# Kernel tuning notes

Measured on AMD Instinct MI355X. Metric: run time of the kernel, lower is better.

Reference implementation:

```python
import jax, jax.numpy as jnp
import numpy as np

MAX_ABS = 1.0          # assumed get_max_abs('T')
DT = 0.01              # forward default dt
TWO_PI = 2.0 * np.pi
B, D, N = 4096, 2048, 4096


def setup_inputs() -> dict:
    key = jax.random.key(0)
    k0, k1 = jax.random.split(key, 2)
    x = jax.random.normal(k0, (B, D), dtype=jnp.float32)
    # nn.Linear params
    W = jax.random.normal(k1, (N, D), dtype=jnp.float32) * (1.0 / np.sqrt(D))
    b = jnp.zeros((N,), dtype=jnp.float32)
    # oscillator params (as initialized in __init__)
    amplitude = jnp.ones((N,), dtype=jnp.float32)
    frequency = jnp.ones((N,), dtype=jnp.float32)
    phase_offset = jnp.zeros((N,), dtype=jnp.float32)
    damping = jnp.full((N,), 0.01, dtype=jnp.float32)
    return {"x": x, "W": W, "b": b, "amplitude": amplitude,
            "frequency": frequency, "phase_offset": phase_offset,
            "damping": damping}


def reference(x, W, b, amplitude, frequency, phase_offset, damping):
    # driving force: [B, N]
    force = x @ W.T + b
    omega_sq = (TWO_PI * frequency) ** 2  # [N]
    # t starts at 0 and is incremented ONCE per forward call
    t = DT

    def step(carry, f):
        state, vel = carry
        accel = -omega_sq * state - damping * vel + f
        vel = vel + accel * DT
        state = state + vel * DT
        return (state, vel), state

    init = (jnp.zeros((N,), x.dtype), jnp.zeros((N,), x.dtype))
    (_, _), states = jax.lax.scan(step, init, force)  # states: [B, N]

    # sinusoid term is identical for every batch step (t fixed within forward)
    osc = amplitude * jnp.sin(TWO_PI * frequency * t + phase_offset)  # [N]
    out = jnp.clip(states + osc, -MAX_ABS, MAX_ABS)
    return out
```

## Files before the change

### kernel.cpp

```cpp
#include <hip/hip_runtime.h>
#include <hip/hip_bf16.h>
#include <math.h>

#define MDIM 4096
#define KDIM 2048
#define NDIM 4096
#define DT   0.01f
#define TWO_PI_F 6.283185307179586f
#define CH 64
#define CL 64

typedef __attribute__((ext_vector_type(8))) short bf16x8;
typedef __attribute__((ext_vector_type(4))) float f32x4;

__device__ __forceinline__ unsigned short f2bf(float f) {
  unsigned int u = __float_as_uint(f);
  u += 0x7FFFu + ((u >> 16) & 1u);
  return (unsigned short)(u >> 16);
}
__device__ __forceinline__ float bf2f(unsigned short u) {
  return __uint_as_float(((unsigned int)u) << 16);
}

__global__ void cast2_bf16_kernel(const float* __restrict__ s0,
                                  unsigned short* __restrict__ d0,
                                  const float* __restrict__ s1,
                                  unsigned short* __restrict__ d1,
                                  int n4each) {
  int i = blockIdx.x * blockDim.x + threadIdx.x;
  const float4* sp;
  ushort4* dp;
  int j;
  if (i < n4each) { sp = (const float4*)s0; dp = (ushort4*)d0; j = i; }
  else            { sp = (const float4*)s1; dp = (ushort4*)d1; j = i - n4each; }
  float4 v = sp[j];
  ushort4 o;
  o.x = f2bf(v.x); o.y = f2bf(v.y); o.z = f2bf(v.z); o.w = f2bf(v.w);
  dp[j] = o;
}

__global__ __launch_bounds__(256, 2) void gemm_bt_kernel(
    const unsigned short* __restrict__ A,
    const unsigned short* __restrict__ Bm,
    const float* __restrict__ bias,
    unsigned short* __restrict__ C) {
  __shared__ __align__(16) unsigned short sA[128 * 32];
  __shared__ __align__(16) unsigned short sB[128 * 32];

  const int tid  = threadIdx.x;
  const int lane = tid & 63;
  const int wave = tid >> 6;
  const int wr = wave >> 1;
  const int wc = wave & 1;
  const int q  = lane >> 4;
  const int lm = lane & 15;

  const int bM = blockIdx.x * 128;
  const int bN = blockIdx.y * 128;

  f32x4 acc[4][4];
#pragma unroll
  for (int i = 0; i < 4; i++)
#pragma unroll
    for (int j = 0; j < 4; j++) acc[i][j] = (f32x4){0.f, 0.f, 0.f, 0.f};

  const int idx0 = tid;
  const int idx1 = tid + 256;
  const int r0 = idx0 >> 2, g0 = idx0 & 3;
  const int r1 = idx1 >> 2, g1 = idx1 & 3;
  const int dst0 = r0 * 32 + ((g0 ^ ((r0 >> 1) & 3)) * 8);
  const int dst1 = r1 * 32 + ((g1 ^ ((r1 >> 1) & 3)) * 8);
  const unsigned short* gA0 = A  + (size_t)(bM + r0) * KDIM + g0 * 8;
  const unsigned short* gA1 = A  + (size_t)(bM + r1) * KDIM + g1 * 8;
  const unsigned short* gB0 = Bm + (size_t)(bN + r0) * KDIM + g0 * 8;
  const unsigned short* gB1 = Bm + (size_t)(bN + r1) * KDIM + g1 * 8;

  const int rq = (q ^ ((lm >> 1) & 3)) * 8;

  for (int k0 = 0; k0 < KDIM; k0 += 32) {
    uint4 av0 = *(const uint4*)(gA0 + k0);
    uint4 av1 = *(const uint4*)(gA1 + k0);
    uint4 bv0 = *(const uint4*)(gB0 + k0);
    uint4 bv1 = *(const uint4*)(gB1 + k0);
    __syncthreads();
    *(uint4*)&sA[dst0] = av0;
    *(uint4*)&sA[dst1] = av1;
    *(uint4*)&sB[dst0] = bv0;
    *(uint4*)&sB[dst1] = bv1;
    __syncthreads();

    bf16x8 af[4], bfr[4];
#pragma unroll
    for (int mt = 0; mt < 4; mt++)
      af[mt]  = *(const bf16x8*)&sA[(wr * 64 + mt * 16 + lm) * 32 + rq];
#pragma unroll
    for (int nt = 0; nt < 4; nt++)
      bfr[nt] = *(const bf16x8*)&sB[(wc * 64 + nt * 16 + lm) * 32 + rq];

#pragma unroll
    for (int mt = 0; mt < 4; mt++)
#pragma unroll
      for (int nt = 0; nt < 4; nt++)
        acc[mt][nt] = __builtin_amdgcn_mfma_f32_16x16x32_bf16(
            af[mt], bfr[nt], acc[mt][nt], 0, 0, 0);
  }

#pragma unroll
  for (int nt = 0; nt < 4; nt++) {
    const int col = bN + wc * 64 + nt * 16 + lm;
    const float bz = bias[col];
#pragma unroll
    for (int mt = 0; mt < 4; mt++) {
      const int row0 = bM + wr * 64 + mt * 16 + q * 4;
#pragma unroll
      for (int r = 0; r < 4; r++)
        C[(size_t)(row0 + r) * NDIM + col] = f2bf(acc[mt][nt][r] + bz);
    }
  }
}

__global__ void scan_pass1(const unsigned short* __restrict__ force,
                           const float* __restrict__ freq,
                           const float* __restrict__ damp,
                           float* __restrict__ chunkS,
                           float* __restrict__ chunkV) {
  int gid = blockIdx.x * blockDim.x + threadIdx.x;
  int n4 = gid & (NDIM / 4 - 1);
  int c  = gid >> 10;
  int n  = n4 * 4;
  float4 fr = *(const float4*)&freq[n];
  float4 dv = *(const float4*)&damp[n];
  float osq[4] = {TWO_PI_F * fr.x, TWO_PI_F * fr.y, TWO_PI_F * fr.z, TWO_PI_F * fr.w};
  float dp[4]  = {dv.x, dv.y, dv.z, dv.w};
  float s[4] = {0.f, 0.f, 0.f, 0.f}, v[4] = {0.f, 0.f, 0.f, 0.f};
#pragma unroll
  for (int j = 0; j < 4; j++) osq[j] *= osq[j];
  const unsigned short* fp = force + (size_t)c * CL * NDIM + n;
#pragma unroll 4
  for (int i = 0; i < CL; i++) {
    ushort4 fv = *(const ushort4*)&fp[(size_t)i * NDIM];
    float f[4] = {bf2f(fv.x), bf2f(fv.y), bf2f(fv.z), bf2f(fv.w)};
#pragma unroll
    for (int j = 0; j < 4; j++) {
      float a = -osq[j] * s[j] - dp[j] * v[j] + f[j];
      v[j] += a * DT;
      s[j] += v[j] * DT;
    }
  }
  *(float4*)&chunkS[c * NDIM + n] = (float4){s[0], s[1], s[2], s[3]};
  *(float4*)&chunkV[c * NDIM + n] = (float4){v[0], v[1], v[2], v[3]};
}

__global__ void scan_pass2(const float* __restrict__ chunkS,
                           const float* __restrict__ chunkV,
                           const float* __restrict__ freq,
                           const float* __restrict__ damp,
                           float* __restrict__ carryS,
                           float* __restrict__ carryV) {
  int n = blockIdx.x * blockDim.x + threadIdx.x;
  float om = TWO_PI_F * freq[n];
  float osq = om * om;
  float dp = damp[n];
  float a00 = 1.f - osq * DT * DT, a01 = DT * (1.f - dp * DT);
  float a10 = -osq * DT,           a11 = 1.f - dp * DT;
#pragma unroll
  for (int i = 0; i < 6; i++) {
    float b00 = a00 * a00 + a01 * a10;
    float b01 = a00 * a01 + a01 * a11;
    float b10 = a10 * a00 + a11 * a10;
    float b11 = a10 * a01 + a11 * a11;
    a00 = b00; a01 = b01; a10 = b10; a11 = b11;
  }
  float cs = 0.f, cv = 0.f;
#pragma unroll 8
  for (int c = 0; c < CH; c++) {
    carryS[c * NDIM + n] = cs;
    carryV[c * NDIM + n] = cv;
    float ls = chunkS[c * NDIM + n];
    float lv = chunkV[c * NDIM + n];
    float ns = a00 * cs + a01 * cv + ls;
    float nv = a10 * cs + a11 * cv + lv;
    cs = ns; cv = nv;
  }
}

__global__ void scan_pass3(const unsigned short* __restrict__ force,
                           const float* __restrict__ amp,
                           const float* __restrict__ freq,
                           const float* __restrict__ phase,
                           const float* __restrict__ damp,
                           const float* __restrict__ carryS,
                           const float* __restrict__ carryV,
                           float* __restrict__ out) {
  int gid = blockIdx.x * blockDim.x + threadIdx.x;
  int n4 = gid & (NDIM / 4 - 1);
  int c  = gid >> 10;
  int n  = n4 * 4;
  float4 fr = *(const float4*)&freq[n];
  float4 dv = *(const float4*)&damp[n];
  float4 am = *(const float4*)&amp[n];
  float4 ph = *(const float4*)&phase[n];
  float om[4] = {TWO_PI_F * fr.x, TWO_PI_F * fr.y, TWO_PI_F * fr.z, TWO_PI_F * fr.w};
  float dp[4] = {dv.x, dv.y, dv.z, dv.w};
  float osq[4], osc[4], s[4], v[4];
  float amv[4] = {am.x, am.y, am.z, am.w};
  float phv[4] = {ph.x, ph.y, ph.z, ph.w};
#pragma unroll
  for (int j = 0; j < 4; j++) {
    osq[j] = om[j] * om[j];
    osc[j] = amv[j] * sinf(om[j] * DT + phv[j]);
  }
  float4 csv = *(const float4*)&carryS[c * NDIM + n];
  float4 cvv = *(const float4*)&carryV[c * NDIM + n];
  s[0] = csv.x; s[1] = csv.y; s[2] = csv.z; s[3] = csv.w;
  v[0] = cvv.x; v[1] = cvv.y; v[2] = cvv.z; v[3] = cvv.w;
  const unsigned short* fp = force + (size_t)c * CL * NDIM + n;
  float* op = out + (size_t)c * CL * NDIM + n;
#pragma unroll 4
  for (int i = 0; i < CL; i++) {
    ushort4 fv = *(const ushort4*)&fp[(size_t)i * NDIM];
    float f[4] = {bf2f(fv.x), bf2f(fv.y), bf2f(fv.z), bf2f(fv.w)};
    float o[4];
#pragma unroll
    for (int j = 0; j < 4; j++) {
      float a = -osq[j] * s[j] - dp[j] * v[j] + f[j];
      v[j] += a * DT;
      s[j] += v[j] * DT;
      o[j] = fminf(1.f, fmaxf(-1.f, s[j] + osc[j]));
    }
    *(float4*)&op[(size_t)i * NDIM] = (float4){o[0], o[1], o[2], o[3]};
  }
}

extern "C" void kernel_launch(void* const* d_in, const int* in_sizes, int n_in,
                              void* d_out, int out_size, void* d_ws, size_t ws_size,
                              hipStream_t stream) {
  const float* x     = (const float*)d_in[0];
  const float* W     = (const float*)d_in[1];
  const float* bias  = (const float*)d_in[2];
  const float* amp   = (const float*)d_in[3];
  const float* freq  = (const float*)d_in[4];
  const float* phase = (const float*)d_in[5];
  const float* damp  = (const float*)d_in[6];

  unsigned short* xbf   = (unsigned short*)d_ws;
  unsigned short* wbf   = xbf + (size_t)MDIM * KDIM;
  unsigned short* force = wbf + (size_t)NDIM * KDIM;
  float* chunkS = (float*)d_ws;
  float* chunkV = chunkS + CH * NDIM;
  float* carryS = chunkV + CH * NDIM;
  float* carryV = carryS + CH * NDIM;

  const int n4each = MDIM * KDIM / 4;
  cast2_bf16_kernel<<<(2 * n4each + 255) / 256, 256, 0, stream>>>(
      x, xbf, W, wbf, n4each);

  dim3 gg(MDIM / 128, NDIM / 128);
  gemm_bt_kernel<<<gg, 256, 0, stream>>>(xbf, wbf, bias, force);

  scan_pass1<<<CH * NDIM / 4 / 256, 256, 0, stream>>>(force, freq, damp,
                                                      chunkS, chunkV);
  scan_pass2<<<NDIM / 256, 256, 0, stream>>>(chunkS, chunkV, freq, damp,
                                             carryS, carryV);
  scan_pass3<<<CH * NDIM / 4 / 256, 256, 0, stream>>>(
      force, amp, freq, phase, damp, carryS, carryV, (float*)d_out);
}
```

Before: 229.1 us.

## Fuse per-chunk oscillator scan into GEMM epilogue and merge carry pass

The GEMM epilogue now stages each wave's 64x64 tile in shared memory, runs the zero-initial-state oscillator recurrence down each column, and writes the partial states plus chunk-final state and velocity. A single follow-up kernel composes the chunk carries using the 64-step transition matrix, which is built by squaring the one-step matrix six times. It then adds the propagated homogeneous response to the partial states, applies the sinusoid and clips. This drops the separate force pass and the carry kernel, cutting a full read of the force matrix and two launches. The trade-offs are a serial loop in the epilogue, extra bf16 rounding of the partial states, an O(chunk) carry loop per thread, and a dependence on a workspace of at least 66 MiB, with the old path kept as a fallback.

```diff
diff --git a/kernel.cpp b/kernel.cpp
--- a/kernel.cpp
+++ b/kernel.cpp
@@ -39,13 +39,18 @@
   dp[j] = o;
 }
 
-__global__ __launch_bounds__(256, 2) void gemm_bt_kernel(
+__global__ __launch_bounds__(256, 2) void gemm_scan_kernel(
     const unsigned short* __restrict__ A,
     const unsigned short* __restrict__ Bm,
     const float* __restrict__ bias,
-    unsigned short* __restrict__ C) {
-  __shared__ __align__(16) unsigned short sA[128 * 32];
-  __shared__ __align__(16) unsigned short sB[128 * 32];
+    const float* __restrict__ freq,
+    const float* __restrict__ damp,
+    unsigned short* __restrict__ zpart,
+    float* __restrict__ chunkS,
+    float* __restrict__ chunkV) {
+  __shared__ __align__(16) unsigned short smem[16384];
+  unsigned short* sA = smem;
+  unsigned short* sB = smem + 4096;
 
   const int tid  = threadIdx.x;
   const int lane = tid & 63;
@@ -74,7 +79,187 @@
   const unsigned short* gA1 = A  + (size_t)(bM + r1) * KDIM + g1 * 8;
   const unsigned short* gB0 = Bm + (size_t)(bN + r0) * KDIM + g0 * 8;
   const unsigned short* gB1 = Bm + (size_t)(bN + r1) * KDIM + g1 * 8;
-
+  const int rq = (q ^ ((lm >> 1) & 3)) * 8;
+
+  for (int k0 = 0; k0 < KDIM; k0 += 32) {
+    uint4 av0 = *(const uint4*)(gA0 + k0);
+    uint4 av1 = *(const uint4*)(gA1 + k0);
+    uint4 bv0 = *(const uint4*)(gB0 + k0);
+    uint4 bv1 = *(const uint4*)(gB1 + k0);
+    __syncthreads();
+    *(uint4*)&sA[dst0] = av0;
+    *(uint4*)&sA[dst1] = av1;
+    *(uint4*)&sB[dst0] = bv0;
+    *(uint4*)&sB[dst1] = bv1;
+    __syncthreads();
+
+    bf16x8 af[4], bfr[4];
+#pragma unroll
+    for (int mt = 0; mt < 4; mt++)
+      af[mt]  = *(const bf16x8*)&sA[(wr * 64 + mt * 16 + lm) * 32 + rq];
+#pragma unroll
+    for (int nt = 0; nt < 4; nt++)
+      bfr[nt] = *(const bf16x8*)&sB[(wc * 64 + nt * 16 + lm) * 32 + rq];
+
+#pragma unroll
+    for (int mt = 0; mt < 4; mt++)
+#pragma unroll
+      for (int nt = 0; nt < 4; nt++)
+        acc[mt][nt] = __builtin_amdgcn_mfma_f32_16x16x32_bf16(
+            af[mt], bfr[nt], acc[mt][nt], 0, 0, 0);
+  }
+
+  __syncthreads();
+  unsigned short* sT = smem + wave * 4096;
+#pragma unroll
+  for (int nt = 0; nt < 4; nt++) {
+    const float bz = bias[bN + wc * 64 + nt * 16 + lm];
+#pragma unroll
+    for (int mt = 0; mt < 4; mt++)
+#pragma unroll
+      for (int r = 0; r < 4; r++)
+        sT[(mt * 16 + q * 4 + r) * 64 + nt * 16 + lm] =
+            f2bf(acc[mt][nt][r] + bz);
+  }
+  __syncthreads();
+
+  const int gcol = bN + wc * 64 + lane;
+  const float om  = TWO_PI_F * freq[gcol];
+  const float osq = om * om;
+  const float dp  = damp[gcol];
+  float s = 0.f, v = 0.f;
+#pragma unroll 8
+  for (int i = 0; i < CL; i++) {
+    float f = bf2f(sT[i * 64 + lane]);
+    v += (-osq * s - dp * v + f) * DT;
+    s += v * DT;
+    sT[i * 64 + lane] = f2bf(s);
+  }
+  const int chunk = 2 * blockIdx.x + wr;
+  chunkS[chunk * NDIM + gcol] = s;
+  chunkV[chunk * NDIM + gcol] = v;
+  __syncthreads();
+
+#pragma unroll
+  for (int k = 0; k < 8; k++) {
+    int slot = lane + 64 * k;
+    int row  = slot >> 3;
+    int col8 = (slot & 7) * 8;
+    *(uint4*)&zpart[(size_t)(bM + wr * 64 + row) * NDIM + bN + wc * 64 + col8] =
+        *(uint4*)&sT[row * 64 + col8];
+  }
+}
+
+__global__ void scan_out_kernel(const unsigned short* __restrict__ zpart,
+                                const float* __restrict__ amp,
+                                const float* __restrict__ freq,
+                                const float* __restrict__ phase,
+                                const float* __restrict__ damp,
+                                const float* __restrict__ chunkS,
+                                const float* __restrict__ chunkV,
+                                float* __restrict__ out) {
+  int gid = blockIdx.x * blockDim.x + threadIdx.x;
+  int n4 = gid & (NDIM / 4 - 1);
+  int c  = gid >> 10;
+  int n  = n4 * 4;
+
+  float4 fr = *(const float4*)&freq[n];
+  float4 dv = *(const float4*)&damp[n];
+  float4 am = *(const float4*)&amp[n];
+  float4 ph = *(const float4*)&phase[n];
+  float omv[4] = {TWO_PI_F * fr.x, TWO_PI_F * fr.y, TWO_PI_F * fr.z, TWO_PI_F * fr.w};
+  float dpv[4] = {dv.x, dv.y, dv.z, dv.w};
+  float amv[4] = {am.x, am.y, am.z, am.w};
+  float phv[4] = {ph.x, ph.y, ph.z, ph.w};
+  float m00[4], m01[4], m10[4], m11[4];
+  float p00[4], p01[4], p10[4], p11[4];
+  float osc[4];
+#pragma unroll
+  for (int j = 0; j < 4; j++) {
+    float osq = omv[j] * omv[j];
+    m00[j] = 1.f - osq * DT * DT;  m01[j] = DT * (1.f - dpv[j] * DT);
+    m10[j] = -osq * DT;            m11[j] = 1.f - dpv[j] * DT;
+    p00[j] = m00[j]; p01[j] = m01[j]; p10[j] = m10[j]; p11[j] = m11[j];
+    osc[j] = amv[j] * sinf(omv[j] * DT + phv[j]);
+  }
+#pragma unroll
+  for (int i = 0; i < 6; i++)
+#pragma unroll
+    for (int j = 0; j < 4; j++) {
+      float b00 = p00[j] * p00[j] + p01[j] * p10[j];
+      float b01 = p00[j] * p01[j] + p01[j] * p11[j];
+      float b10 = p10[j] * p00[j] + p11[j] * p10[j];
+      float b11 = p10[j] * p01[j] + p11[j] * p11[j];
+      p00[j] = b00; p01[j] = b01; p10[j] = b10; p11[j] = b11;
+    }
+
+  float hs[4] = {0.f, 0.f, 0.f, 0.f}, hv[4] = {0.f, 0.f, 0.f, 0.f};
+  for (int cc = 0; cc < c; cc++) {
+    float4 ls = *(const float4*)&chunkS[cc * NDIM + n];
+    float4 lv = *(const float4*)&chunkV[cc * NDIM + n];
+    float lsv[4] = {ls.x, ls.y, ls.z, ls.w};
+    float lvv[4] = {lv.x, lv.y, lv.z, lv.w};
+#pragma unroll
+    for (int j = 0; j < 4; j++) {
+      float t = p00[j] * hs[j] + p01[j] * hv[j] + lsv[j];
+      float u = p10[j] * hs[j] + p11[j] * hv[j] + lvv[j];
+      hs[j] = t; hv[j] = u;
+    }
+  }
+
+  const unsigned short* zp = zpart + (size_t)c * CL * NDIM + n;
+  float* op = out + (size_t)c * CL * NDIM + n;
+#pragma unroll 4
+  for (int i = 0; i < CL; i++) {
+    ushort4 zv = *(const ushort4*)&zp[(size_t)i * NDIM];
+    float z[4] = {bf2f(zv.x), bf2f(zv.y), bf2f(zv.z), bf2f(zv.w)};
+    float o[4];
+#pragma unroll
+    for (int j = 0; j < 4; j++) {
+      float t = m00[j] * hs[j] + m01[j] * hv[j];
+      float u = m10[j] * hs[j] + m11[j] * hv[j];
+      hs[j] = t; hv[j] = u;
+      o[j] = fminf(1.f, fmaxf(-1.f, hs[j] + z[j] + osc[j]));
+    }
+    *(float4*)&op[(size_t)i * NDIM] = (float4){o[0], o[1], o[2], o[3]};
+  }
+}
+
+__global__ __launch_bounds__(256, 2) void gemm_bt_kernel(
+    const unsigned short* __restrict__ A,
+    const unsigned short* __restrict__ Bm,
+    const float* __restrict__ bias,
+    unsigned short* __restrict__ C) {
+  __shared__ __align__(16) unsigned short sA[128 * 32];
+  __shared__ __align__(16) unsigned short sB[128 * 32];
+
+  const int tid  = threadIdx.x;
+  const int lane = tid & 63;
+  const int wave = tid >> 6;
+  const int wr = wave >> 1;
+  const int wc = wave & 1;
+  const int q  = lane >> 4;
+  const int lm = lane & 15;
+
+  const int bM = blockIdx.x * 128;
+  const int bN = blockIdx.y * 128;
+
+  f32x4 acc[4][4];
+#pragma unroll
+  for (int i = 0; i < 4; i++)
+#pragma unroll
+    for (int j = 0; j < 4; j++) acc[i][j] = (f32x4){0.f, 0.f, 0.f, 0.f};
+
+  const int idx0 = tid;
+  const int idx1 = tid + 256;
+  const int r0 = idx0 >> 2, g0 = idx0 & 3;
+  const int r1 = idx1 >> 2, g1 = idx1 & 3;
+  const int dst0 = r0 * 32 + ((g0 ^ ((r0 >> 1) & 3)) * 8);
+  const int dst1 = r1 * 32 + ((g1 ^ ((r1 >> 1) & 3)) * 8);
+  const unsigned short* gA0 = A  + (size_t)(bM + r0) * KDIM + g0 * 8;
+  const unsigned short* gA1 = A  + (size_t)(bM + r1) * KDIM + g1 * 8;
+  const unsigned short* gB0 = Bm + (size_t)(bN + r0) * KDIM + g0 * 8;
+  const unsigned short* gB1 = Bm + (size_t)(bN + r1) * KDIM + g1 * 8;
   const int rq = (q ^ ((lm >> 1) & 3)) * 8;
 
   for (int k0 = 0; k0 < KDIM; k0 += 32) {
@@ -243,25 +428,40 @@
   const float* phase = (const float*)d_in[5];
   const float* damp  = (const float*)d_in[6];
 
-  unsigned short* xbf   = (unsigned short*)d_ws;
-  unsigned short* wbf   = xbf + (size_t)MDIM * KDIM;
-  unsigned short* force = wbf + (size_t)NDIM * KDIM;
-  float* chunkS = (float*)d_ws;
-  float* chunkV = chunkS + CH * NDIM;
-  float* carryS = chunkV + CH * NDIM;
-  float* carryV = carryS + CH * NDIM;
-
+  const size_t MiB = 1024 * 1024;
   const int n4each = MDIM * KDIM / 4;
-  cast2_bf16_kernel<<<(2 * n4each + 255) / 256, 256, 0, stream>>>(
-      x, xbf, W, wbf, n4each);
-
   dim3 gg(MDIM / 128, NDIM / 128);
-  gemm_bt_kernel<<<gg, 256, 0, stream>>>(xbf, wbf, bias, force);
-
-  scan_pass1<<<CH * NDIM / 4 / 256, 256, 0, stream>>>(force, freq, damp,
-                                                      chunkS, chunkV);
-  scan_pass2<<<NDIM / 256, 256, 0, stream>>>(chunkS, chunkV, freq, damp,
-                                             carryS, carryV);
-  scan_pass3<<<CH * NDIM / 4 / 256, 256, 0, stream>>>(
-      force, amp, freq, phase, damp, carryS, carryV, (float*)d_out);
-}
+
+  if (ws_size >= 66 * MiB) {
+    unsigned short* xbf   = (unsigned short*)d_ws;
+    unsigned short* wbf   = xbf + (size_t)MDIM * KDIM;
+    unsigned short* zpart = wbf + (size_t)NDIM * KDIM;
+    float* chunkS = (float*)((char*)d_ws + 64 * MiB);
+    float* chunkV = chunkS + CH * NDIM;
+
+    cast2_bf16_kernel<<<(2 * n4each + 255) / 256, 256, 0, stream>>>(
+        x, xbf, W, wbf, n4each);
+    gemm_scan_kernel<<<gg, 256, 0, stream>>>(xbf, wbf, bias, freq, damp,
+                                             zpart, chunkS, chunkV);
+    scan_out_kernel<<<CH * NDIM / 4 / 256, 256, 0, stream>>>(
+        zpart, amp, freq, phase, damp, chunkS, chunkV, (float*)d_out);
+  } else {
+    unsigned short* xbf   = (unsigned short*)d_ws;
+    unsigned short* wbf   = xbf + (size_t)MDIM * KDIM;
+    unsigned short* force = wbf + (size_t)NDIM * KDIM;
+    float* chunkS = (float*)d_ws;
+    float* chunkV = chunkS + CH * NDIM;
+    float* carryS = chunkV + CH * NDIM;
+    float* carryV = carryS + CH * NDIM;
+
+    cast2_bf16_kernel<<<(2 * n4each + 255) / 256, 256, 0, stream>>>(
+        x, xbf, W, wbf, n4each);
+    gemm_bt_kernel<<<gg, 256, 0, stream>>>(xbf, wbf, bias, force);
+    scan_pass1<<<CH * NDIM / 4 / 256, 256, 0, stream>>>(force, freq, damp,
+                                                        chunkS, chunkV);
+    scan_pass2<<<NDIM / 256, 256, 0, stream>>>(chunkS, chunkV, freq, damp,
+                                               carryS, carryV);
+    scan_pass3<<<CH * NDIM / 4 / 256, 256, 0, stream>>>(
+        force, amp, freq, phase, damp, carryS, carryV, (float*)d_out);
+  }
+}
```

New measurement: 236.4 us. 1.03x slower.
